# Kernel tuning notes

Hardware: AMD Instinct MI355X
Metric: run time of the kernel (lower is better)

Reference implementation:

```python
import jax, jax.numpy as jnp
import numpy as np

NUM_DAYS = 365

# ---- physics model stand-in (SegmentPhysicsModel.compute_current) ----
# source repo not available; use a simple photovoltaic current law:
# I = G * ISC_REF * (1 + ALPHA*(Tcell - T_REF)), channels 0/1 of raw_features.
ISC_REF = 9.0
ALPHA = 0.0005
T_REF = 0.5

def _physics_current(raw):
    G = raw[..., 0:1]
    Tc = raw[..., 1:2]
    return G * ISC_REF * (1.0 + ALPHA * (Tc - T_REF))  # [B,T,1]


def _lstm_layer(x, Wih, Whh, bih, bhh):
    # x: [B,T,D]; PyTorch gate order i,f,g,o
    B = x.shape[0]
    H = Whh.shape[1]
    def step(carry, xt):
        h, c = carry
        g = xt @ Wih.T + h @ Whh.T + bih + bhh
        i, f, gg, o = jnp.split(g, 4, axis=-1)
        c = jax.nn.sigmoid(f) * c + jax.nn.sigmoid(i) * jnp.tanh(gg)
        h = jax.nn.sigmoid(o) * jnp.tanh(c)
        return (h, c), h
    h0 = jnp.zeros((B, H), x.dtype)
    c0 = jnp.zeros((B, H), x.dtype)
    _, ys = jax.lax.scan(step, (h0, c0), jnp.swapaxes(x, 0, 1))
    return jnp.swapaxes(ys, 0, 1)  # [B,T,H]


def _ode_trajectory(h0, W1, b1, W2, b2, W3, b3):
    # dopri5 tableau, fixed step over the t=linspace(0,1,num_days+1) grid
    dt = 1.0 / NUM_DAYS
    def f(h, t):
        inp = jnp.concatenate([h, jnp.reshape(t, (1,))])
        z = jnp.tanh(inp @ W1.T + b1)
        z = jnp.tanh(z @ W2.T + b2)
        return z @ W3.T + b3
    def step(h, t):
        k1 = f(h, t)
        k2 = f(h + dt * (1/5) * k1, t + dt * (1/5))
        k3 = f(h + dt * (3/40 * k1 + 9/40 * k2), t + dt * (3/10))
        k4 = f(h + dt * (44/45 * k1 - 56/15 * k2 + 32/9 * k3), t + dt * (4/5))
        k5 = f(h + dt * (19372/6561 * k1 - 25360/2187 * k2 + 64448/6561 * k3 - 212/729 * k4), t + dt * (8/9))
        k6 = f(h + dt * (9017/3168 * k1 - 355/33 * k2 + 46732/5247 * k3 + 49/176 * k4 - 5103/18656 * k5), t + dt)
        hn = h + dt * (35/384 * k1 + 500/1113 * k3 + 125/192 * k4 - 2187/6784 * k5 + 11/84 * k6)
        return hn, hn
    times = jnp.linspace(0.0, 1.0, NUM_DAYS + 1, dtype=h0.dtype)
    _, traj = jax.lax.scan(step, h0, times[:-1])
    return jnp.concatenate([h0[None, :], traj], axis=0)  # [num_days+1, H]


def setup_inputs() -> dict:
    key = jax.random.key(0)
    ks = jax.random.split(key, 32)
    B, T, F, Fraw = 256, 2048, 32, 4
    HID, HD, FH = 64, 8, 64
    n = lambda k, s, sc=0.05: (jax.random.normal(k, s, dtype=jnp.float32) * sc)
    inp = {
        "X": jax.random.normal(ks[0], (B, T, F), dtype=jnp.float32),
        "day_ids": jax.random.randint(ks[1], (B,), 0, NUM_DAYS + 1),
        "raw_features": jax.random.uniform(ks[2], (B, T, Fraw), dtype=jnp.float32),
        "initial_health": n(ks[3], (HD,), 0.1),
        "ode_W1": n(ks[4], (64, HD + 1)), "ode_b1": jnp.zeros((64,), jnp.float32),
        "ode_W2": n(ks[5], (64, 64)), "ode_b2": jnp.zeros((64,), jnp.float32),
        "ode_W3": n(ks[6], (HD, 64)), "ode_b3": jnp.zeros((HD,), jnp.float32),
        "lstm_Wih0": n(ks[7], (4 * HID, F)), "lstm_Whh0": n(ks[8], (4 * HID, HID)),
        "lstm_bih0": jnp.zeros((4 * HID,), jnp.float32), "lstm_bhh0": jnp.zeros((4 * HID,), jnp.float32),
        "lstm_Wih1": n(ks[9], (4 * HID, HID)), "lstm_Whh1": n(ks[10], (4 * HID, HID)),
        "lstm_bih1": jnp.zeros((4 * HID,), jnp.float32), "lstm_bhh1": jnp.zeros((4 * HID,), jnp.float32),
        "head_decay_weight": n(ks[11], (HD,), 0.01), "head_decay_bias": jnp.zeros((1,), jnp.float32),
        "fus_W1": n(ks[12], (FH, HID + HD + 1)), "fus_b1": jnp.zeros((FH,), jnp.float32),
        "fus_W2": n(ks[13], (FH, FH)), "fus_b2": jnp.zeros((FH,), jnp.float32),
        "res_W1": n(ks[14], (FH // 2, FH)), "res_b1": jnp.zeros((FH // 2,), jnp.float32),
        "res_W2": n(ks[15], (1, FH // 2)), "res_b2": jnp.zeros((1,), jnp.float32),
    }
    return inp


def reference(X, day_ids, raw_features, initial_health, ode_W1, ode_b1, ode_W2, ode_b2, ode_W3, ode_b3, lstm_Wih0, lstm_Whh0, lstm_bih0, lstm_bhh0, lstm_Wih1, lstm_Whh1, lstm_bih1, lstm_bhh1, head_decay_weight, head_decay_bias, fus_W1, fus_b1, fus_W2, fus_b2, res_W1, res_b1, res_W2, res_b2):
    B, T, _ = X.shape
    # LSTM encoder (2 layers)
    env_seq = _lstm_layer(X, lstm_Wih0, lstm_Whh0, lstm_bih0, lstm_bhh0)
    env_seq = _lstm_layer(env_seq, lstm_Wih1, lstm_Whh1, lstm_bih1, lstm_bhh1)
    # health table is detached (traj.detach()) in the original -> stop_gradient
    traj = jax.lax.stop_gradient(_ode_trajectory(initial_health, ode_W1, ode_b1, ode_W2, ode_b2, ode_W3, ode_b3))
    health = traj[day_ids]                                   # [B, H]
    health_seq = jnp.broadcast_to(health[:, None, :], (B, T, health.shape[-1]))
    raw_D = jnp.sum(health_seq * head_decay_weight, axis=-1, keepdims=True) + head_decay_bias
    D = jax.nn.sigmoid(raw_D)                                # [B,T,1]
    I_phys = _physics_current(raw_features)                  # [B,T,1]
    I_base = D * I_phys
    z = jnp.concatenate([env_seq, health_seq, I_phys], axis=-1)  # [B,T,73]
    feat = jax.nn.relu(z @ fus_W1.T + fus_b1)
    feat = jax.nn.relu(feat @ fus_W2.T + fus_b2)
    r = jax.nn.relu(feat @ res_W1.T + res_b1) @ res_W2.T + res_b2
    I_pred = I_base + r
    return (I_pred, I_phys, I_base, D, r, health_seq)
```

## Files before the change

### kernel.cpp

```cpp
#include <hip/hip_runtime.h>
#include <hip/hip_bf16.h>
#include <cstdint>
#include <cstddef>

typedef unsigned int uint;
typedef unsigned short ushort;
typedef _Float16 half2_t __attribute__((ext_vector_type(2)));

#define BATCH 256
#define SEQT  2048
#define FIN   32
#define HID   64
#define FH    64
#define NTOT  (BATCH*SEQT)

enum : int {
  O_B0   = 0,
  O_B1   = O_B0 + 256,
  O_OW1  = O_B1 + 256,
  O_OB1  = O_OW1 + 64*9,
  O_OW2  = O_OB1 + 64,
  O_OB2  = O_OW2 + 64*64,
  O_OW3  = O_OB2 + 64,
  O_OB3  = O_OW3 + 8*64,
  O_OH0  = O_OB3 + 8,
  O_FW1  = O_OH0 + 8,
  O_FB1  = O_FW1 + 64*73,
  O_FW2  = O_FB1 + 64,
  O_FB2  = O_FW2 + 64*64,
  O_RW1  = O_FB2 + 64,
  O_RB1  = O_RW1 + 32*64,
  O_RW2  = O_RB1 + 32,
  O_RB2  = O_RW2 + 32,
  O_HW   = O_RB2 + 1,
  O_HB   = O_HW + 8,
  O_TRAJ = O_HB + 1,
  WS_F32_END = O_TRAJ + 366*8,
  H_WIH0 = WS_F32_END,
  H_WHH0 = H_WIH0 + 256*16,
  H_WIH1 = H_WHH0 + 256*32,
  H_WHH1 = H_WIH1 + 256*32,
  WS_END2 = H_WHH1 + 256*32
};

#define O_FLAG_BYTE  (500*1024)
#define ENV_BYTE_OFF (512*1024)

__device__ __forceinline__ float blo(uint u){ return __uint_as_float(u<<16); }
__device__ __forceinline__ float bhi(uint u){ return __uint_as_float(u & 0xffff0000u); }
__device__ __forceinline__ ushort f2b(float x){
  uint u = __float_as_uint(x);
  uint r = u + 0x7fffu + ((u>>16)&1u);
  return (ushort)(r>>16);
}
__device__ __forceinline__ float sigm(float x){ return 1.0f/(1.0f+__expf(-x)); }
__device__ __forceinline__ float tanh_fast(float x){
  x = fminf(10.0f, fmaxf(-10.0f, x));
  float e = __expf(-2.0f*x);
  return (1.0f - e)/(1.0f + e);
}
__device__ __forceinline__ void wsync(){
  __builtin_amdgcn_wave_barrier();
  __threadfence_block();
  __builtin_amdgcn_wave_barrier();
}
__device__ __forceinline__ uint pkh2(float a, float b){
  half2_t h; h.x=(_Float16)a; h.y=(_Float16)b;
  return __builtin_bit_cast(uint, h);
}
__device__ __forceinline__ half2_t uph(uint u){ return __builtin_bit_cast(half2_t, u); }
__device__ __forceinline__ int hbits(float x){
  return (int)__builtin_bit_cast(ushort, (_Float16)x) & 0xFFFF;
}
#define WAIT_LGKM0() __builtin_amdgcn_s_waitcnt(0xC07F)
#define MEMBAR()     asm volatile("" ::: "memory")

#if __has_builtin(__builtin_amdgcn_fdot2)
__device__ __forceinline__ float FDOT2(uint a, uint b, float c){
  return __builtin_amdgcn_fdot2(uph(a), uph(b), c, false);
}
#else
__device__ __forceinline__ float FDOT2(uint a, uint b, float c){
  half2_t x = uph(a), y = uph(b);
  return c + (float)x.x*(float)y.x + (float)x.y*(float)y.y;
}
#endif

__global__ void detect_kernel(const uint* __restrict__ X, int* __restrict__ flagp) {
  if (threadIdx.x == 0) {
    int cnt = 0;
    for (int i=0;i<512;i++){
      uint e = (X[i]>>23)&0xFFu;
      cnt += (e>=97u && e<=157u) ? 1 : 0;
    }
    *flagp = (cnt >= 300) ? 1 : 0;
  }
}

struct Ptrs { const void* p[28]; };

__global__ void prep_kernel(Ptrs ptrs, float* __restrict__ ws, const int* __restrict__ flagp) {
  const int flag = *flagp;
  const int tid = blockIdx.x*blockDim.x + threadIdx.x;
  const int nth = gridDim.x*blockDim.x;
  auto cv = [&](int dst, int srcidx, int n){
    if (flag) {
      const float* s = (const float*)ptrs.p[srcidx];
      for (int i=tid;i<n;i+=nth) ws[dst+i] = s[i];
    } else {
      const ushort* s = (const ushort*)ptrs.p[srcidx];
      for (int i=tid;i<n;i+=nth) ws[dst+i] = __uint_as_float(((uint)s[i])<<16);
    }
  };
  auto rd = [&](int srcidx, int i)->float{
    if (flag) return ((const float*)ptrs.p[srcidx])[i];
    return __uint_as_float(((uint)((const ushort*)ptrs.p[srcidx])[i])<<16);
  };
  auto cvh = [&](int dstw, int srcidx, int n2){
    uint* d = (uint*)ws;
    if (flag) {
      const float* s = (const float*)ptrs.p[srcidx];
      for (int i=tid;i<n2;i+=nth) d[dstw+i] = pkh2(s[2*i], s[2*i+1]);
    } else {
      const uint* s = (const uint*)ptrs.p[srcidx];
      for (int i=tid;i<n2;i+=nth){ uint u=s[i]; d[dstw+i] = pkh2(blo(u), bhi(u)); }
    }
  };
  cvh(H_WIH0,10,4096); cvh(H_WHH0,11,8192); cvh(H_WIH1,14,8192); cvh(H_WHH1,15,8192);
  for (int i=tid;i<256;i+=nth) ws[O_B0+i] = rd(12,i) + rd(13,i);
  for (int i=tid;i<256;i+=nth) ws[O_B1+i] = rd(16,i) + rd(17,i);
  cv(O_OW1,4,576); cv(O_OB1,5,64); cv(O_OW2,6,4096); cv(O_OB2,7,64);
  cv(O_OW3,8,512); cv(O_OB3,9,8);  cv(O_OH0,3,8);
  cv(O_FW1,20,4672); cv(O_FB1,21,64); cv(O_FW2,22,4096); cv(O_FB2,23,64);
  cv(O_RW1,24,2048); cv(O_RB1,25,32); cv(O_RW2,26,32); cv(O_RB2,27,1);
  cv(O_HW,18,8); cv(O_HB,19,1);
}

__device__ void ode_wave(float* __restrict__ ws, float* sbuf) {
  const int lane = threadIdx.x;
  float* sZ1 = sbuf;
  float* sZ2 = sbuf + 64;
  float* sK  = sbuf + 128;

  float w1[9];
#pragma unroll
  for (int k=0;k<9;k++) w1[k]=ws[O_OW1+lane*9+k];
  const float b1 = ws[O_OB1+lane];
  float w2[64];
#pragma unroll
  for (int k=0;k<64;k++) w2[k]=ws[O_OW2+lane*64+k];
  const float b2 = ws[O_OB2+lane];
  const int m = lane>>3, s = lane&7;
  float w3[8];
#pragma unroll
  for (int k=0;k<8;k++) w3[k]=ws[O_OW3+m*64+s*8+k];
  const float b3m = ws[O_OB3+m];

  float h[8];
#pragma unroll
  for (int k=0;k<8;k++) h[k]=ws[O_OH0+k];

  {
    float sel = h[0];
#pragma unroll
    for (int i=1;i<8;i++) sel = (lane==i)? h[i] : sel;
    if (lane<8) ws[O_TRAJ+lane]=sel;
  }

  const float dt = 1.0f/365.0f;
  float k1[8],k2[8],k3[8],k4[8],k5[8],k6[8],ht[8];

  auto feval = [&](const float* hin, float te, float* kout) {
    float a = b1;
#pragma unroll
    for (int k=0;k<8;k++) a += w1[k]*hin[k];
    a += w1[8]*te;
    sZ1[lane] = tanh_fast(a);
    wsync();
    float acc = b2;
    {
      const float4* z4 = (const float4*)sZ1;
#pragma unroll
      for (int k=0;k<16;k++){ float4 v=z4[k];
        acc += w2[4*k]*v.x + w2[4*k+1]*v.y + w2[4*k+2]*v.z + w2[4*k+3]*v.w; }
    }
    sZ2[lane] = tanh_fast(acc);
    wsync();
    float part;
    {
      const float4* q = (const float4*)(sZ2 + s*8);
      float4 p0=q[0], p1=q[1];
      part = w3[0]*p0.x + w3[1]*p0.y + w3[2]*p0.z + w3[3]*p0.w
           + w3[4]*p1.x + w3[5]*p1.y + w3[6]*p1.z + w3[7]*p1.w;
    }
    part += __shfl_xor(part, 1);
    part += __shfl_xor(part, 2);
    part += __shfl_xor(part, 4);
    if (s==0) sK[m] = part + b3m;
    wsync();
    {
      const float4* kk = (const float4*)sK;
      float4 a0=kk[0], a1=kk[1];
      kout[0]=a0.x; kout[1]=a0.y; kout[2]=a0.z; kout[3]=a0.w;
      kout[4]=a1.x; kout[5]=a1.y; kout[6]=a1.z; kout[7]=a1.w;
    }
    wsync();
  };

  for (int d=0; d<365; d++) {
    float t0 = (float)d * dt;
    feval(h, t0, k1);
#pragma unroll
    for (int i=0;i<8;i++) ht[i] = h[i] + dt*(0.2f*k1[i]);
    feval(ht, t0 + 0.2f*dt, k2);
#pragma unroll
    for (int i=0;i<8;i++) ht[i] = h[i] + dt*((3.0f/40.0f)*k1[i] + (9.0f/40.0f)*k2[i]);
    feval(ht, t0 + 0.3f*dt, k3);
#pragma unroll
    for (int i=0;i<8;i++) ht[i] = h[i] + dt*((44.0f/45.0f)*k1[i] - (56.0f/15.0f)*k2[i] + (32.0f/9.0f)*k3[i]);
    feval(ht, t0 + 0.8f*dt, k4);
#pragma unroll
    for (int i=0;i<8;i++) ht[i] = h[i] + dt*((19372.0f/6561.0f)*k1[i] - (25360.0f/2187.0f)*k2[i]
                                   + (64448.0f/6561.0f)*k3[i] - (212.0f/729.0f)*k4[i]);
    feval(ht, t0 + (8.0f/9.0f)*dt, k5);
#pragma unroll
    for (int i=0;i<8;i++) ht[i] = h[i] + dt*((9017.0f/3168.0f)*k1[i] - (355.0f/33.0f)*k2[i]
                                   + (46732.0f/5247.0f)*k3[i] + (49.0f/176.0f)*k4[i]
                                   - (5103.0f/18656.0f)*k5[i]);
    feval(ht, t0 + dt, k6);
#pragma unroll
    for (int i=0;i<8;i++) h[i] += dt*((35.0f/384.0f)*k1[i] + (500.0f/1113.0f)*k3[i]
                                   + (125.0f/192.0f)*k4[i] - (2187.0f/6784.0f)*k5[i]
                                   + (11.0f/84.0f)*k6[i]);
    float sel = h[0];
#pragma unroll
    for (int i=1;i<8;i++) sel = (lane==i)? h[i] : sel;
    if (lane<8) ws[O_TRAJ + (d+1)*8 + lane] = sel;
  }
}

#define RH 64
#define RP 16

__global__ __launch_bounds__(192) void lstm_pipe_kernel(const void* __restrict__ Xv,
                                                        float* __restrict__ ws,
                                                        ushort* __restrict__ env,
                                                        const int* __restrict__ flagp,
                                                        int b0, int runOde, int nb) {
  __shared__ __align__(16) uint  sx[128*16];
  __shared__ __align__(16) uint  ringH[RH*32];
  __shared__ __align__(16) float ringP[RP*256];
  __shared__ int cnts[4];

  if ((int)blockIdx.x == nb) {
    if (runOde && threadIdx.x < 64) ode_wave(ws, (float*)sx);
    return;
  }

  const int flag = *flagp;
  const int b = b0 + blockIdx.x;
  const int wave = threadIdx.x >> 6;
  const int lane = threadIdx.x & 63;
  const uint* wsu = (const uint*)ws;
  if (threadIdx.x < 4) cnts[threadIdx.x] = -1;
  __syncthreads();
  volatile int* vc = cnts;

  if (wave == 0) {
    uint wx[4][16], wh[4][32];
    float bias[4];
#pragma unroll
    for (int g=0; g<4; g++){
      const uint4* p = (const uint4*)(wsu + H_WIH0 + (g*64+lane)*16);
#pragma unroll
      for (int q=0;q<4;q++){ uint4 v=p[q]; wx[g][4*q]=v.x; wx[g][4*q+1]=v.y; wx[g][4*q+2]=v.z; wx[g][4*q+3]=v.w; }
      const uint4* r = (const uint4*)(wsu + H_WHH0 + (g*64+lane)*32);
#pragma unroll
      for (int q=0;q<8;q++){ uint4 v=r[q]; wh[g][4*q]=v.x; wh[g][4*q+1]=v.y; wh[g][4*q+2]=v.z; wh[g][4*q+3]=v.w; }
      bias[g] = ws[O_B0 + g*64 + lane];
    }
    const uint4*   xb4 = (const uint4*)((const uint*)Xv + (size_t)b*SEQT*16);
    const float4*  xf4 = (const float4*)((const float*)Xv + (size_t)b*SEQT*FIN);
    float c1 = 0.0f;
    uint vh1pk = 0u;

    for (int t=0; t<SEQT; ++t) {
      if ((t & 127) == 0) {
        if (flag) {
#pragma unroll
          for (int i=0;i<16;i++){
            float4 v = xf4[(size_t)(t>>2)*8  + i*64 + lane];
            uint2 w; w.x = pkh2(v.x,v.y); w.y = pkh2(v.z,v.w);
            ((uint2*)sx)[i*64 + lane] = w;
          }
        } else {
#pragma unroll
          for (int i=0;i<8;i++){
            uint4 u = xb4[(size_t)t*4 + i*64 + lane];
            uint4 w;
            w.x = pkh2(blo(u.x), bhi(u.x)); w.y = pkh2(blo(u.y), bhi(u.y));
            w.z = pkh2(blo(u.z), bhi(u.z)); w.w = pkh2(blo(u.w), bhi(u.w));
            ((uint4*)sx)[i*64 + lane] = w;
          }
        }
      }
      while (vc[1] < t - RH) { __builtin_amdgcn_s_sleep(1); }

      uint vx = sx[(t&127)*16 + (lane&15)];
      float a[4] = {bias[0], bias[1], bias[2], bias[3]};
      float z[4] = {0.f,0.f,0.f,0.f};
#pragma unroll
      for (int k=0;k<16;k++){
        uint s = (uint)__builtin_amdgcn_readlane((int)vx, k);
        if (k&1){ z[0]=FDOT2(wx[0][k],s,z[0]); z[1]=FDOT2(wx[1][k],s,z[1]);
                  z[2]=FDOT2(wx[2][k],s,z[2]); z[3]=FDOT2(wx[3][k],s,z[3]); }
        else    { a[0]=FDOT2(wx[0][k],s,a[0]); a[1]=FDOT2(wx[1][k],s,a[1]);
                  a[2]=FDOT2(wx[2][k],s,a[2]); a[3]=FDOT2(wx[3][k],s,a[3]); }
      }
#pragma unroll
      for (int k=0;k<32;k++){
        uint s = (uint)__builtin_amdgcn_readlane((int)vh1pk, k);
        if (k&1){ z[0]=FDOT2(wh[0][k],s,z[0]); z[1]=FDOT2(wh[1][k],s,z[1]);
                  z[2]=FDOT2(wh[2][k],s,z[2]); z[3]=FDOT2(wh[3][k],s,z[3]); }
        else    { a[0]=FDOT2(wh[0][k],s,a[0]); a[1]=FDOT2(wh[1][k],s,a[1]);
                  a[2]=FDOT2(wh[2][k],s,a[2]); a[3]=FDOT2(wh[3][k],s,a[3]); }
      }
      float gi=a[0]+z[0], gf=a[1]+z[1], gg=a[2]+z[2], go=a[3]+z[3];
      c1 = sigm(gf)*c1 + sigm(gi)*tanh_fast(gg);
      float h1 = sigm(go)*tanh_fast(c1);
      int hb = hbits(h1);
      uint lo = (uint)__shfl(hb, 2*lane);
      uint hi = (uint)__shfl(hb, 2*lane+1);
      vh1pk = lo | (hi<<16);
      if (lane < 32) ringH[(t&(RH-1))*32 + lane] = vh1pk;
      WAIT_LGKM0(); MEMBAR();
      if (lane == 0) vc[0] = t;
    }
  } else if (wave == 1) {
    uint wi[4][32];
    float bias1[4];
#pragma unroll
    for (int g=0; g<4; g++){
      const uint4* p = (const uint4*)(wsu + H_WIH1 + (g*64+lane)*32);
#pragma unroll
      for (int q=0;q<8;q++){ uint4 v=p[q]; wi[g][4*q]=v.x; wi[g][4*q+1]=v.y; wi[g][4*q+2]=v.z; wi[g][4*q+3]=v.w; }
      bias1[g] = ws[O_B1 + g*64 + lane];
    }
    for (int t=0; t<SEQT; ++t) {
      while (vc[0] < t)      { __builtin_amdgcn_s_sleep(1); }
      while (vc[2] < t - RP) { __builtin_amdgcn_s_sleep(1); }
      MEMBAR();
      uint vh = ringH[(t&(RH-1))*32 + (lane&31)];
      float p0=bias1[0], p1=bias1[1], p2=bias1[2], p3=bias1[3];
      float q0=0.f, q1=0.f, q2=0.f, q3=0.f;
#pragma unroll
      for (int k=0;k<32;k++){
        uint s = (uint)__builtin_amdgcn_readlane((int)vh, k);
        if (k&1){ q0=FDOT2(wi[0][k],s,q0); q1=FDOT2(wi[1][k],s,q1);
                  q2=FDOT2(wi[2][k],s,q2); q3=FDOT2(wi[3][k],s,q3); }
        else    { p0=FDOT2(wi[0][k],s,p0); p1=FDOT2(wi[1][k],s,p1);
                  p2=FDOT2(wi[2][k],s,p2); p3=FDOT2(wi[3][k],s,p3); }
      }
      ((float4*)(ringP + (t&(RP-1))*256))[lane] = make_float4(p0+q0, p1+q1, p2+q2, p3+q3);
      WAIT_LGKM0(); MEMBAR();
      if (lane == 0) vc[1] = t;
    }
  } else {
    uint wh2[4][32];
#pragma unroll
    for (int g=0; g<4; g++){
      const uint4* p = (const uint4*)(wsu + H_WHH1 + (g*64+lane)*32);
#pragma unroll
      for (int q=0;q<8;q++){ uint4 v=p[q]; wh2[g][4*q]=v.x; wh2[g][4*q+1]=v.y; wh2[g][4*q+2]=v.z; wh2[g][4*q+3]=v.w; }
    }
    uint* erow = (uint*)env + (size_t)blockIdx.x*SEQT*32;
    float c2 = 0.0f;
    uint vh2pk = 0u;
    for (int t=0; t<SEQT; ++t) {
      while (vc[1] < t) { __builtin_amdgcn_s_sleep(1); }
      MEMBAR();
      float4 pp = ((const float4*)(ringP + (t&(RP-1))*256))[lane];
      float a0=0.f,a1=0.f,a2=0.f,a3=0.f, z0=0.f,z1=0.f,z2=0.f,z3=0.f;
#pragma unroll
      for (int k=0;k<32;k++){
        uint s = (uint)__builtin_amdgcn_readlane((int)vh2pk, k);
        if (k&1){ z0=FDOT2(wh2[0][k],s,z0); z1=FDOT2(wh2[1][k],s,z1);
                  z2=FDOT2(wh2[2][k],s,z2); z3=FDOT2(wh2[3][k],s,z3); }
        else    { a0=FDOT2(wh2[0][k],s,a0); a1=FDOT2(wh2[1][k],s,a1);
                  a2=FDOT2(wh2[2][k],s,a2); a3=FDOT2(wh2[3][k],s,a3); }
      }
      float gi=pp.x+a0+z0, gf=pp.y+a1+z1, gg=pp.z+a2+z2, go=pp.w+a3+z3;
      c2 = sigm(gf)*c2 + sigm(gi)*tanh_fast(gg);
      float h2 = sigm(go)*tanh_fast(c2);
      int hb = hbits(h2);
      uint lo = (uint)__shfl(hb, 2*lane);
      uint hi = (uint)__shfl(hb, 2*lane+1);
      vh2pk = lo | (hi<<16);
      if (lane < 32) erow[(size_t)t*32 + lane] = vh2pk;
      WAIT_LGKM0(); MEMBAR();
      if (lane == 0) vc[2] = t;
    }
  }
}

__global__ __launch_bounds__(256) void fuse_kernel(const ushort* __restrict__ envb,
                                                   const float* __restrict__ ws,
                                                   const int* __restrict__ day_ids,
                                                   const void* __restrict__ rawv,
                                                   void* __restrict__ outv,
                                                   const int* __restrict__ flagp,
                                                   int b0, int nb) {
  const int flag = *flagp;
  const int eloc = blockIdx.x*256 + threadIdx.x;
  const int bloc = eloc >> 11;
  const int b = b0 + bloc;
  const size_t ge = (size_t)b*SEQT + (eloc & 2047);

  int day = day_ids[b];
  day = day < 0 ? 0 : (day > 365 ? 365 : day);
  float hl[8];
#pragma unroll
  for (int i=0;i<8;i++) hl[i] = ws[O_TRAJ + day*8 + i];
  float rawD = ws[O_HB];
#pragma unroll
  for (int i=0;i<8;i++) rawD += hl[i]*ws[O_HW+i];
  const float Dv = sigm(rawD);

  float z[HID];
  {
    const uint4* ev = (const uint4*)(envb + (size_t)eloc*HID);
#pragma unroll
    for (int q=0;q<8;q++){
      uint4 u = ev[q];
      half2_t h0=uph(u.x), h1=uph(u.y), h2=uph(u.z), h3=uph(u.w);
      z[8*q+0]=(float)h0.x; z[8*q+1]=(float)h0.y;
      z[8*q+2]=(float)h1.x; z[8*q+3]=(float)h1.y;
      z[8*q+4]=(float)h2.x; z[8*q+5]=(float)h2.y;
      z[8*q+6]=(float)h3.x; z[8*q+7]=(float)h3.y;
    }
  }
  float G, Tc;
  if (flag) {
    float2 fr = ((const float2*)rawv)[ge*2];
    G = fr.x; Tc = fr.y;
  } else {
    uint gr = ((const uint*)rawv)[ge*2];
    G = blo(gr); Tc = bhi(gr);
  }
  const float Ip = G*9.0f*(1.0f + 0.0005f*(Tc-0.5f));

  float f1[FH];
#pragma unroll
  for (int jj=0;jj<FH;jj++){
    const float* wr = ws + O_FW1 + jj*73;
    float a = ws[O_FB1+jj];
#pragma unroll
    for (int k=0;k<HID;k++) a += wr[k]*z[k];
#pragma unroll
    for (int i=0;i<8;i++) a += wr[HID+i]*hl[i];
    a += wr[72]*Ip;
    f1[jj] = fmaxf(a,0.0f);
  }
  float f2[FH];
#pragma unroll
  for (int jj=0;jj<FH;jj++){
    const float* wr = ws + O_FW2 + jj*FH;
    float a = ws[O_FB2+jj];
#pragma unroll
    for (int k=0;k<FH;k++) a += wr[k]*f1[k];
    f2[jj] = fmaxf(a,0.0f);
  }
  float racc = ws[O_RB2];
#pragma unroll
  for (int mm=0;mm<32;mm++){
    const float* wr = ws + O_RW1 + mm*FH;
    float a = ws[O_RB1+mm];
#pragma unroll
    for (int k=0;k<FH;k++) a += wr[k]*f2[k];
    racc += ws[O_RW2+mm]*fmaxf(a,0.0f);
  }
  const float Ib = Dv*Ip;
  const float Ipred = Ib + racc;

  if (flag) {
    float* o = (float*)outv;
    o[ge] = Ipred; o[NTOT+ge] = Ip; o[(size_t)2*NTOT+ge] = Ib;
    o[(size_t)3*NTOT+ge] = Dv; o[(size_t)4*NTOT+ge] = racc;
    float4* hp = (float4*)(o + (size_t)5*NTOT + ge*8);
    hp[0] = make_float4(hl[0],hl[1],hl[2],hl[3]);
    hp[1] = make_float4(hl[4],hl[5],hl[6],hl[7]);
  } else {
    ushort* o = (ushort*)outv;
    o[ge] = f2b(Ipred); o[NTOT+ge] = f2b(Ip); o[(size_t)2*NTOT+ge] = f2b(Ib);
    o[(size_t)3*NTOT+ge] = f2b(Dv); o[(size_t)4*NTOT+ge] = f2b(racc);
    uint4 hsv;
    hsv.x = (uint)f2b(hl[0]) | ((uint)f2b(hl[1])<<16);
    hsv.y = (uint)f2b(hl[2]) | ((uint)f2b(hl[3])<<16);
    hsv.z = (uint)f2b(hl[4]) | ((uint)f2b(hl[5])<<16);
    hsv.w = (uint)f2b(hl[6]) | ((uint)f2b(hl[7])<<16);
    *((uint4*)(o + (size_t)5*NTOT + ge*8)) = hsv;
  }
}

extern "C" void kernel_launch(void* const* d_in, const int* in_sizes, int n_in,
                              void* d_out, int out_size, void* d_ws, size_t ws_size,
                              hipStream_t stream) {
  (void)in_sizes; (void)out_size;
  float* wsf = (float*)d_ws;
  int* flagp = (int*)((char*)d_ws + O_FLAG_BYTE);
  ushort* env = (ushort*)((char*)d_ws + ENV_BYTE_OFF);
  Ptrs pa;
  for (int i=0;i<28;i++) pa.p[i] = (i<n_in) ? d_in[i] : d_in[0];

  int S = 1;
  while (S < 128) {
    size_t need = (size_t)ENV_BYTE_OFF + (size_t)(BATCH/S)*SEQT*HID*2;
    if (need <= ws_size) break;
    S <<= 1;
  }
  const int nb = BATCH / S;

  detect_kernel<<<1, 64, 0, stream>>>((const uint*)d_in[0], flagp);
  prep_kernel<<<128, 256, 0, stream>>>(pa, wsf, flagp);
  for (int s=0; s<S; s++) {
    lstm_pipe_kernel<<<nb+1, 192, 0, stream>>>(d_in[0], wsf, env, flagp,
                                               s*nb, (s==0)?1:0, nb);
    fuse_kernel<<<nb*(SEQT/256), 256, 0, stream>>>(env, wsf, (const int*)d_in[1],
                                                   d_in[2], d_out, flagp, s*nb, nb);
  }
}
```

Measured before the change: 2.425 ms.

## Batch LSTM inter-wave handshakes every four steps and fold ODE into a fourth wave

The three-wave LSTM pipeline now publishes its progress counters and polls them only once per group of four timesteps, instead of every step. The slack on the ring buffers is adjusted to match. This removes most per-step LDS waits, memory barriers and spin-polls from the serial recurrence. The ODE solve moves from an extra block to a fourth wave of block 0. The fp32 input-load index is also corrected, and input rows are now fetched four timesteps at a time. In exchange, the consumer waves lag further behind and the ring headroom is tighter.

```diff
diff --git a/kernel.cpp b/kernel.cpp
--- a/kernel.cpp
+++ b/kernel.cpp
@@ -137,7 +137,7 @@
 }
 
 __device__ void ode_wave(float* __restrict__ ws, float* sbuf) {
-  const int lane = threadIdx.x;
+  const int lane = threadIdx.x & 63;
   float* sZ1 = sbuf;
   float* sZ2 = sbuf + 64;
   float* sK  = sbuf + 128;
@@ -242,29 +242,31 @@
 #define RH 64
 #define RP 16
 
-__global__ __launch_bounds__(192) void lstm_pipe_kernel(const void* __restrict__ Xv,
-                                                        float* __restrict__ ws,
-                                                        ushort* __restrict__ env,
-                                                        const int* __restrict__ flagp,
-                                                        int b0, int runOde, int nb) {
+__global__ __launch_bounds__(256, 1) void lstm_pipe_kernel(const void* __restrict__ Xv,
+                                                           float* __restrict__ ws,
+                                                           ushort* __restrict__ env,
+                                                           const int* __restrict__ flagp,
+                                                           int b0, int runOde) {
   __shared__ __align__(16) uint  sx[128*16];
   __shared__ __align__(16) uint  ringH[RH*32];
   __shared__ __align__(16) float ringP[RP*256];
+  __shared__ __align__(16) float odebuf[192];
   __shared__ int cnts[4];
 
-  if ((int)blockIdx.x == nb) {
-    if (runOde && threadIdx.x < 64) ode_wave(ws, (float*)sx);
-    return;
-  }
-
-  const int flag = *flagp;
-  const int b = b0 + blockIdx.x;
   const int wave = threadIdx.x >> 6;
   const int lane = threadIdx.x & 63;
-  const uint* wsu = (const uint*)ws;
   if (threadIdx.x < 4) cnts[threadIdx.x] = -1;
   __syncthreads();
   volatile int* vc = cnts;
+
+  if (wave == 3) {
+    if (runOde && blockIdx.x == 0) ode_wave(ws, odebuf);
+    return;
+  }
+
+  const int flag = *flagp;
+  const int b = b0 + blockIdx.x;
+  const uint* wsu = (const uint*)ws;
 
   if (wave == 0) {
     uint wx[4][16], wh[4][32];
@@ -283,13 +285,14 @@
     const float4*  xf4 = (const float4*)((const float*)Xv + (size_t)b*SEQT*FIN);
     float c1 = 0.0f;
     uint vh1pk = 0u;
+    uint vxq = 0u;
 
     for (int t=0; t<SEQT; ++t) {
       if ((t & 127) == 0) {
         if (flag) {
 #pragma unroll
           for (int i=0;i<16;i++){
-            float4 v = xf4[(size_t)(t>>2)*8  + i*64 + lane];
+            float4 v = xf4[(size_t)t*8 + i*64 + lane];
             uint2 w; w.x = pkh2(v.x,v.y); w.y = pkh2(v.z,v.w);
             ((uint2*)sx)[i*64 + lane] = w;
           }
@@ -304,14 +307,18 @@
           }
         }
       }
-      while (vc[1] < t - RH) { __builtin_amdgcn_s_sleep(1); }
-
-      uint vx = sx[(t&127)*16 + (lane&15)];
+      const int s4 = t & 3;
+      if (s4 == 0) {
+        while (vc[1] < t - 56) { __builtin_amdgcn_s_sleep(1); }
+        MEMBAR();
+        vxq = sx[((t + (lane>>4)) & 127)*16 + (lane&15)];
+      }
       float a[4] = {bias[0], bias[1], bias[2], bias[3]};
       float z[4] = {0.f,0.f,0.f,0.f};
+      const int sb = s4 << 4;
 #pragma unroll
       for (int k=0;k<16;k++){
-        uint s = (uint)__builtin_amdgcn_readlane((int)vx, k);
+        uint s = (uint)__builtin_amdgcn_readlane((int)vxq, sb + k);
         if (k&1){ z[0]=FDOT2(wx[0][k],s,z[0]); z[1]=FDOT2(wx[1][k],s,z[1]);
                   z[2]=FDOT2(wx[2][k],s,z[2]); z[3]=FDOT2(wx[3][k],s,z[3]); }
         else    { a[0]=FDOT2(wx[0][k],s,a[0]); a[1]=FDOT2(wx[1][k],s,a[1]);
@@ -333,8 +340,10 @@
       uint hi = (uint)__shfl(hb, 2*lane+1);
       vh1pk = lo | (hi<<16);
       if (lane < 32) ringH[(t&(RH-1))*32 + lane] = vh1pk;
-      WAIT_LGKM0(); MEMBAR();
-      if (lane == 0) vc[0] = t;
+      if (s4 == 3) {
+        WAIT_LGKM0(); MEMBAR();
+        if (lane == 0) vc[0] = t;
+      }
     }
   } else if (wave == 1) {
     uint wi[4][32];
@@ -347,9 +356,11 @@
       bias1[g] = ws[O_B1 + g*64 + lane];
     }
     for (int t=0; t<SEQT; ++t) {
-      while (vc[0] < t)      { __builtin_amdgcn_s_sleep(1); }
-      while (vc[2] < t - RP) { __builtin_amdgcn_s_sleep(1); }
-      MEMBAR();
+      if ((t & 3) == 0) {
+        while (vc[0] < t + 3) { __builtin_amdgcn_s_sleep(1); }
+        while (vc[2] < t - 8) { __builtin_amdgcn_s_sleep(1); }
+        MEMBAR();
+      }
       uint vh = ringH[(t&(RH-1))*32 + (lane&31)];
       float p0=bias1[0], p1=bias1[1], p2=bias1[2], p3=bias1[3];
       float q0=0.f, q1=0.f, q2=0.f, q3=0.f;
@@ -362,8 +373,10 @@
                   p2=FDOT2(wi[2][k],s,p2); p3=FDOT2(wi[3][k],s,p3); }
       }
       ((float4*)(ringP + (t&(RP-1))*256))[lane] = make_float4(p0+q0, p1+q1, p2+q2, p3+q3);
-      WAIT_LGKM0(); MEMBAR();
-      if (lane == 0) vc[1] = t;
+      if ((t & 3) == 3) {
+        WAIT_LGKM0(); MEMBAR();
+        if (lane == 0) vc[1] = t;
+      }
     }
   } else {
     uint wh2[4][32];
@@ -377,8 +390,10 @@
     float c2 = 0.0f;
     uint vh2pk = 0u;
     for (int t=0; t<SEQT; ++t) {
-      while (vc[1] < t) { __builtin_amdgcn_s_sleep(1); }
-      MEMBAR();
+      if ((t & 3) == 0) {
+        while (vc[1] < t + 3) { __builtin_amdgcn_s_sleep(1); }
+        MEMBAR();
+      }
       float4 pp = ((const float4*)(ringP + (t&(RP-1))*256))[lane];
       float a0=0.f,a1=0.f,a2=0.f,a3=0.f, z0=0.f,z1=0.f,z2=0.f,z3=0.f;
 #pragma unroll
@@ -397,8 +412,10 @@
       uint hi = (uint)__shfl(hb, 2*lane+1);
       vh2pk = lo | (hi<<16);
       if (lane < 32) erow[(size_t)t*32 + lane] = vh2pk;
-      WAIT_LGKM0(); MEMBAR();
-      if (lane == 0) vc[2] = t;
+      if ((t & 3) == 3) {
+        WAIT_LGKM0(); MEMBAR();
+        if (lane == 0) vc[2] = t;
+      }
     }
   }
 }
@@ -523,8 +540,8 @@
   detect_kernel<<<1, 64, 0, stream>>>((const uint*)d_in[0], flagp);
   prep_kernel<<<128, 256, 0, stream>>>(pa, wsf, flagp);
   for (int s=0; s<S; s++) {
-    lstm_pipe_kernel<<<nb+1, 192, 0, stream>>>(d_in[0], wsf, env, flagp,
-                                               s*nb, (s==0)?1:0, nb);
+    lstm_pipe_kernel<<<nb, 256, 0, stream>>>(d_in[0], wsf, env, flagp,
+                                             s*nb, (s==0)?1:0);
     fuse_kernel<<<nb*(SEQT/256), 256, 0, stream>>>(env, wsf, (const int*)d_in[1],
                                                    d_in[2], d_out, flagp, s*nb, nb);
   }
```

Result: slower. 2.533 ms (+4.5%).
